# Kernel tuning notes

Hardware: AMD Instinct MI355X
Metric: run time of the kernel (lower is better)

Reference implementation:

```python
import jax, jax.numpy as jnp
import numpy as np

PRE = 2000          # pre_wbf_detections
POST = 300          # post_wbf_detections
IOU_THRESH = 0.55   # wbf_iou_thresh
NUM_CLASSES = 5


def setup_inputs() -> dict:
    key = jax.random.key(0)
    k1, k2, k3, k4 = jax.random.split(key, 4)
    # realistic xyxy boxes in a 1024px image
    ctr = jax.random.uniform(k1, (PRE, 2), minval=0.0, maxval=1024.0)
    wh = jax.random.uniform(k2, (PRE, 2), minval=8.0, maxval=96.0)
    boxes = jnp.concatenate([ctr - wh / 2, ctr + wh / 2], axis=1)
    scores = jax.random.uniform(k3, (PRE, 1), minval=0.05, maxval=1.0)
    labels = jax.random.randint(k4, (PRE, 1), 0, NUM_CLASSES).astype(jnp.float32)
    x = jnp.concatenate([boxes, scores, labels], axis=1)  # (PRE, 6)
    return {"x": x}


def _iou_one_vs_many(box, mboxes):
    # torchvision-style box_iou of one box (4,) vs many (N,4)
    lt = jnp.maximum(box[:2], mboxes[:, :2])
    rb = jnp.minimum(box[2:], mboxes[:, 2:])
    wh = jnp.clip(rb - lt, 0.0)
    inter = wh[:, 0] * wh[:, 1]
    a1 = (box[2] - box[0]) * (box[3] - box[1])
    a2 = (mboxes[:, 2] - mboxes[:, 0]) * (mboxes[:, 3] - mboxes[:, 1])
    union = a1 + a2 - inter
    safe = jnp.where(union > 0, union, 1.0)
    return jnp.where(union > 0, inter / safe, 0.0)


def _wbf_forward(x):
    # Sequential WBF clustering. The torch code runs wbf() per unique class;
    # since a detection can only join a cluster of its own class and cluster
    # creation order within a class is preserved, a single sequential pass
    # with a class-equality check is mathematically identical (final result
    # is sorted by score, so per-class concatenation order is irrelevant).
    N = x.shape[0]
    # cluster state: score-weighted box sum, score sum, member count, class, valid
    init = (
        jnp.zeros((N, 4), x.dtype),   # sum of score*box per cluster
        jnp.zeros((N,), x.dtype),     # sum of scores per cluster
        jnp.zeros((N,), jnp.int32),   # member count per cluster
        jnp.zeros((N,), x.dtype),     # class id per cluster
        jnp.zeros((N,), bool),        # cluster slot valid
    )

    def step(carry, det):
        sum_wb, sum_s, cnt, cls, valid = carry
        box, score, c = det[:4], det[4], det[5]
        denom = jnp.where(valid, sum_s, 1.0)
        mboxes = sum_wb / denom[:, None]  # current merged boxes
        iou = _iou_one_vs_many(box, mboxes)
        match = valid & (cls == c) & (iou > IOU_THRESH)
        found = jnp.any(match)
        first = jnp.argmax(match)                  # first matching cluster
        n_valid = jnp.sum(valid).astype(jnp.int32)  # next free slot
        idx = jnp.where(found, first, n_valid)
        sum_wb = sum_wb.at[idx].add(score * box)
        sum_s = sum_s.at[idx].add(score)
        cnt = cnt.at[idx].add(1)
        cls = cls.at[idx].set(c)
        valid = valid.at[idx].set(True)
        return (sum_wb, sum_s, cnt, cls, valid), None

    (sum_wb, sum_s, cnt, cls, valid), _ = jax.lax.scan(step, init, x)

    denom = jnp.where(valid, sum_s, 1.0)
    boxes = sum_wb / denom[:, None]                              # weighted avg box
    scores = sum_s / jnp.maximum(cnt.astype(x.dtype), 1.0)       # mean score
    sort_key = jnp.where(valid, scores, -1.0)
    order = jnp.argsort(-sort_key)                               # descending by score
    top = order[:POST]
    vtop = valid[top]
    out = jnp.concatenate(
        [boxes[top], scores[top, None], cls[top, None]], axis=1)  # (POST, 6)
    return jnp.where(vtop[:, None], out, 0.0)


def reference(x):
    return _wbf_forward(x[:PRE])
```

## Files before the change

kernel.cpp:

```cpp
#include <hip/hip_runtime.h>

typedef unsigned long long u64;
typedef unsigned short u16;
typedef unsigned u32;
typedef unsigned char u8;

#define PRE   2000
#define POST  300
#define NCLS  5
#define CAP   512
#define INF   0x7fffffff
#define SORTG 8

#define MID 0x1.19999A8p-1

template <int K> struct IC { static constexpr int v = K; };
template <int N, typename F> __device__ __forceinline__ void unrollN(F&& f) {
    if constexpr (N > 0) { unrollN<N - 1>(f); f(IC<N - 1>{}); }
}

__device__ __forceinline__ float rlF(float v, int l) {
    return __uint_as_float((u32)__builtin_amdgcn_readlane((int)__float_as_uint(v), l));
}

__device__ __forceinline__ bool iou_pred(float bx0, float bx1, float bx2, float bx3,
                                         float a1, float m0, float m1, float m2, float m3,
                                         float a2) {
    const float ltx = fmaxf(bx0, m0), lty = fmaxf(bx1, m1);
    const float rbx = fminf(bx2, m2), rby = fminf(bx3, m3);
    const float wd = fmaxf(rbx - ltx, 0.f), hg = fmaxf(rby - lty, 0.f);
    const float inter = wd * hg;
    const float uni = (a1 + a2) - inter;
    return (uni > 0.f) && ((double)inter >= MID * (double)uni);
}

__device__ __forceinline__ u64 mk_key(float sc, int g, int id) {
    return ~(((u64)__float_as_uint(sc) << 32) |
             ((u64)(unsigned)(0xFFFF - g) << 16) | (u64)id);
}

__global__ __launch_bounds__(512, 1) void wbf_matrix(const float* __restrict__ x,
                                                     u64* __restrict__ M,
                                                     float* __restrict__ dets,
                                                     int* __restrict__ nlist,
                                                     u64* __restrict__ keysg,
                                                     u32* __restrict__ histg) {
#pragma clang fp contract(off)
    __shared__ int s_wc[8];
    __shared__ u16 s_list[CAP];

    const int tid  = threadIdx.x;
    const int lane = tid & 63;
    const int wave = tid >> 6;
    const int b    = blockIdx.x;
    const int cls  = b >> 4;
    const float mycls = (float)cls;

    if (b == 1) for (int i = tid; i < NCLS * CAP; i += 512) keysg[i] = ~0ull;
    if (b == 2) for (int i = tid; i < 4096; i += 512) histg[i] = 0u;

    u64 wm[4]; int wcnt = 0;
    const int tb = wave * 256;
    #pragma unroll
    for (int i = 0; i < 4; ++i) {
        const int t = tb + i * 64 + lane;
        const bool pp = (t < PRE) && (x[t * 6 + 5] == mycls);
        wm[i] = __ballot(pp);
        wcnt += (int)__popcll(wm[i]);
    }
    if (lane == 0) s_wc[wave] = wcnt;
    __syncthreads();
    int off = 0, tot = 0;
    #pragma unroll
    for (int w = 0; w < 8; ++w) {
        const int cw = s_wc[w];
        off += (w < wave) ? cw : 0;
        tot += cw;
    }
    #pragma unroll
    for (int i = 0; i < 4; ++i) {
        const int t = tb + i * 64 + lane;
        const bool pp = ((wm[i] >> lane) & 1ull) != 0ull;
        const int pos = off + (int)__popcll(wm[i] & (((u64)1 << lane) - 1ull));
        if (pp && pos < CAP) s_list[pos] = (u16)t;
        off += (int)__popcll(wm[i]);
    }
    const int myn = (tot > CAP) ? CAP : tot;
    __syncthreads();

    {
        float qc0[8], qc1[8], qc2[8], qc3[8], ac[8];
        unrollN<8>([&](auto k_) {
            constexpr int K = decltype(k_)::v;
            const int c = K * 64 + lane;
            qc0[K] = 0.f; qc1[K] = 0.f; qc2[K] = 0.f; qc3[K] = 0.f; ac[K] = 0.f;
            if (c < myn) {
                const int g = s_list[c];
                const float* p = x + g * 6;
                const float b0 = p[0], b1 = p[1], b2 = p[2], b3 = p[3], sc = p[4];
                qc0[K] = (sc * b0) / sc; qc1[K] = (sc * b1) / sc;
                qc2[K] = (sc * b2) / sc; qc3[K] = (sc * b3) / sc;
                ac[K] = (qc2[K] - qc0[K]) * (qc3[K] - qc1[K]);
            }
        });
        const int slice = (b & 15) * 8 + wave;
        const int rlo = slice * 4;
        const int rhi = (rlo + 4 < myn) ? rlo + 4 : myn;
        const int nr = rhi - rlo;
        if (nr > 0) {
            float rv0 = 0.f, rv1 = 0.f, rv2 = 0.f, rv3 = 0.f;
            if (lane < nr) {
                const int g = s_list[rlo + lane];
                const float* p = x + g * 6;
                rv0 = p[0]; rv1 = p[1]; rv2 = p[2]; rv3 = p[3];
            }
            for (int i = 0; i < nr; ++i) {
                const int r = rlo + i;
                const float bx0 = rlF(rv0, i), bx1 = rlF(rv1, i);
                const float bx2 = rlF(rv2, i), bx3 = rlF(rv3, i);
                const float a1 = (bx2 - bx0) * (bx3 - bx1);
                const int Wmax = r >> 6;
                unrollN<8>([&](auto w_) {
                    constexpr int W = decltype(w_)::v;
                    if (W <= Wmax) {
                        const int c = W * 64 + lane;
                        const bool pred = (c < r) &&
                            iou_pred(bx0, bx1, bx2, bx3, a1, qc0[W], qc1[W], qc2[W], qc3[W], ac[W]);
                        const u64 bits = __ballot(pred);
                        if (lane == 0) M[((size_t)(cls * CAP + r)) * 8 + W] = bits;
                    }
                });
            }
        }
    }

    if ((b & 15) == 0) {
        for (int rr = tid; rr < myn; rr += 512) {
            const int g = s_list[rr];
            const float* p = x + g * 6;
            const float b0 = p[0], b1 = p[1], b2 = p[2], b3 = p[3], sc = p[4];
            float* dr = dets + (size_t)(cls * CAP + rr) * 8;
            dr[0] = b0; dr[1] = b1; dr[2] = b2; dr[3] = b3;
            dr[4] = sc; dr[5] = (b2 - b0) * (b3 - b1);
            ((int*)dr)[6] = g; ((int*)dr)[7] = 0;
        }
        if (tid == 0) nlist[cls] = myn;
    }
}

__global__ __launch_bounds__(512, 1) void wbf_scan(const u64* __restrict__ M,
                                                   const float* __restrict__ dets,
                                                   const int* __restrict__ nlist,
                                                   float* __restrict__ recs,
                                                   int* __restrict__ cnts,
                                                   u64* __restrict__ keysg,
                                                   u32* __restrict__ histg) {
#pragma clang fp contract(off)
    __shared__ __align__(16) char s_buf[57408];
    u8*  s_mtx = (u8*)s_buf;
    float (*s_det)[8]  = (float (*)[8])(s_buf + 32768);
    float (*s_dov)[16] = (float (*)[16])(s_buf + 49152);
    u8*  s_ab          = (u8*)(s_buf + 57344);

    const int tid  = threadIdx.x;
    const int lane = tid & 63;
    const int wave = tid >> 6;
    const int cls  = blockIdx.x;

    const int myn = nlist[cls];

    {
        const ulonglong2* Mg = (const ulonglong2*)(M + (size_t)cls * CAP * 8);
        ulonglong2* Ml = (ulonglong2*)s_mtx;
        const int nit = myn * 4;
        for (int it = tid; it < nit; it += 512) Ml[it] = Mg[it];
    }
    {
        const float4* Dg = (const float4*)(dets + (size_t)cls * CAP * 8);
        float4* Dl = (float4*)s_det;
        const int nit = myn * 2;
        for (int it = tid; it < nit; it += 512) Dl[it] = Dg[it];
    }
    if (tid < 64) s_ab[tid] = 0;
    __syncthreads();
    if (wave != 0) return;

    u32 aliveB = 0;
    int dirtyCnt = 0;
    bool consA = false;
    int resCode = 0, resIdx = 0;
    float dR0 = 0.f, dR1 = 0.f, dR2 = 0.f, dR3 = 0.f, dRa = 0.f;
    float dS0 = 0.f, dS1 = 0.f, dS2 = 0.f, dS3 = 0.f, dSs = 0.f;
    int dRank = INF, dGi = 0, dCnt = 0;
    float rm0 = 0.f, rm1 = 0.f, rm2 = 0.f, rm3 = 0.f, rma = 0.f;

    auto resolve = [&](int r, float bx0, float bx1, float bx2, float bx3,
                       float sc, float a1, u32 rowByte, u64 balC) {
        const u32 mC = rowByte & aliveB;
        int rank_c = INF;
        if (balC) {
            const int wl = (int)__builtin_ctzll(balC);
            const u32 byte = (u32)__builtin_amdgcn_readlane((int)mC, wl);
            rank_c = wl * 8 + (int)__builtin_ctz(byte);
        }
        const int rcs = (rank_c == INF) ? 0 : rank_c;
        const float4 cbv = *(const float4*)&s_det[rcs][0];
        const float4 cbe = *(const float4*)&s_det[rcs][4];
        const float cb0 = cbv.x, cb1 = cbv.y, cb2 = cbv.z, cb3 = cbv.w;
        const float csc = cbe.x;
        const int cgi = __float_as_int(cbe.z);

        int rank_d = INF, di = -1;
        if (dirtyCnt > 0) {
            const int DN = (dirtyCnt < 64) ? dirtyCnt : 64;
            const bool p = (lane < DN) &&
                iou_pred(bx0, bx1, bx2, bx3, a1, dR0, dR1, dR2, dR3, dRa);
            const int myrk = p ? dRank : INF;
            u64 mk = __ballot(p);
            while (mk) {
                const int l = (int)__builtin_ctzll(mk);
                mk &= mk - 1;
                const int rk = __builtin_amdgcn_readlane(myrk, l);
                if (rk < rank_d) { rank_d = rk; di = l; }
            }
            const int DH2 = (dirtyCnt < 128) ? dirtyCnt : 128;
            for (int dd = 64; dd < DH2; ++dd) {
                const float* dv = s_dov[dd];
                if (iou_pred(bx0, bx1, bx2, bx3, a1, dv[0], dv[1], dv[2], dv[3], dv[4])) {
                    const int rk = ((const int*)dv)[10];
                    if (rk < rank_d) { rank_d = rk; di = dd; }
                }
            }
        }
        if (rank_c == INF && rank_d == INF) {
            aliveB |= ((r >> 3) == lane) ? (1u << (r & 7)) : 0u;
            resCode = 0;
        } else if (rank_c < rank_d) {
            const int rc = rank_c;
            aliveB &= ~(((rc >> 3) == lane) ? (1u << (rc & 7)) : 0u);
            const float ns0 = (csc * cb0) + sc * bx0;
            const float ns1 = (csc * cb1) + sc * bx1;
            const float ns2 = (csc * cb2) + sc * bx2;
            const float ns3 = (csc * cb3) + sc * bx3;
            const float nss = csc + sc;
            const float nm0 = ns0 / nss, nm1 = ns1 / nss;
            const float nm2 = ns2 / nss, nm3 = ns3 / nss;
            const float nar = (nm2 - nm0) * (nm3 - nm1);
            const int D = dirtyCnt;
            if (D < 64) {
                if (lane == D) {
                    dR0 = nm0; dR1 = nm1; dR2 = nm2; dR3 = nm3; dRa = nar;
                    dS0 = ns0; dS1 = ns1; dS2 = ns2; dS3 = ns3; dSs = nss;
                    dRank = rc; dGi = cgi; dCnt = 2;
                }
            } else if (D < 128) {
                if (lane == 0) {
                    float* dv = s_dov[D];
                    dv[0] = nm0; dv[1] = nm1; dv[2] = nm2; dv[3] = nm3; dv[4] = nar;
                    dv[5] = ns0; dv[6] = ns1; dv[7] = ns2; dv[8] = ns3; dv[9] = nss;
                    ((int*)dv)[10] = rc; ((int*)dv)[11] = cgi; ((int*)dv)[12] = 2;
                }
            }
            dirtyCnt++;
            resCode = 1; resIdx = D;
            rm0 = nm0; rm1 = nm1; rm2 = nm2; rm3 = nm3; rma = nar;
        } else {
            float f0, f1, f2, f3, fs; int nct;
            if (di < 64) {
                f0 = rlF(dS0, di) + sc * bx0; f1 = rlF(dS1, di) + sc * bx1;
                f2 = rlF(dS2, di) + sc * bx2; f3 = rlF(dS3, di) + sc * bx3;
                fs = rlF(dSs, di) + sc;
                nct = __builtin_amdgcn_readlane(dCnt, di) + 1;
            } else {
                const float* dv = s_dov[di];
                f0 = dv[5] + sc * bx0; f1 = dv[6] + sc * bx1;
                f2 = dv[7] + sc * bx2; f3 = dv[8] + sc * bx3;
                fs = dv[9] + sc;
                nct = ((const int*)dv)[12] + 1;
            }
            const float nm0 = f0 / fs, nm1 = f1 / fs, nm2 = f2 / fs, nm3 = f3 / fs;
            const float nar = (nm2 - nm0) * (nm3 - nm1);
            if (di < 64) {
                if (lane == di) {
                    dR0 = nm0; dR1 = nm1; dR2 = nm2; dR3 = nm3; dRa = nar;
                    dS0 = f0; dS1 = f1; dS2 = f2; dS3 = f3; dSs = fs; dCnt = nct;
                }
            } else {
                if (lane == 0) {
                    float* dw = s_dov[di];
                    dw[0] = nm0; dw[1] = nm1; dw[2] = nm2; dw[3] = nm3; dw[4] = nar;
                    dw[5] = f0; dw[6] = f1; dw[7] = f2; dw[8] = f3; dw[9] = fs;
                    ((int*)dw)[12] = nct;
                }
            }
            rm0 = nm0; rm1 = nm1; rm2 = nm2; rm3 = nm3; rma = nar;
            resCode = 2; resIdx = di;
        }
    };

    for (int K8 = 0; K8 < 8; ++K8) {
        const int r0 = K8 * 64;
        if (r0 >= myn) break;
        const int cnt = (myn - r0 < 64) ? (myn - r0) : 64;
        const bool valid = lane < cnt;
        const u64 validM = (cnt == 64) ? ~0ull : (((u64)1 << cnt) - 1ull);
        u64 orv = 0ull;
        {
            const int rr = r0 + (valid ? lane : 0);
            const u64* rp = (const u64*)&s_mtx[(size_t)rr * 64];
            const u64* av = (const u64*)s_ab;
            #pragma unroll
            for (int W = 0; W < 8; ++W) {
                if (W <= K8) {
                    const u64 msk = (W == K8) ? ~0ull : av[W];
                    orv |= rp[W] & msk;
                }
            }
        }
        const u64 rowW = __ballot(valid && orv != 0ull);
        float4 db = make_float4(0.f, 0.f, 0.f, 0.f);
        float2 de = make_float2(1.f, 0.f);
        if (valid) {
            db = *(const float4*)&s_det[r0 + lane][0];
            de = *(const float2*)&s_det[r0 + lane][4];
        }
        u64 dmaskLo = 0ull, dmaskHi = 0ull;
        if (!consA) {
            const int DN = (dirtyCnt < 64) ? dirtyCnt : 64;
            for (int d = 0; d < DN; ++d) {
                const float m0 = rlF(dR0, d), m1 = rlF(dR1, d);
                const float m2 = rlF(dR2, d), m3 = rlF(dR3, d);
                const float ma = rlF(dRa, d);
                const bool pp = valid && iou_pred(db.x, db.y, db.z, db.w, de.y,
                                                 m0, m1, m2, m3, ma);
                if (pp) dmaskLo |= 1ull << d;
            }
            const int DH = (dirtyCnt < 128) ? dirtyCnt : 128;
            for (int dd = 64; dd < DH; ++dd) {
                const float* dv = s_dov[dd];
                const bool pp = valid && iou_pred(db.x, db.y, db.z, db.w, de.y,
                                                 dv[0], dv[1], dv[2], dv[3], dv[4]);
                if (pp) dmaskHi |= 1ull << (dd - 64);
            }
        }
        u64 danyb = __ballot((dmaskLo | dmaskHi) != 0ull);

        u32 prB[8]; int prP[8];
        {
            u64 t = consA ? validM : ((danyb | rowW) & validM);
            #pragma unroll
            for (int i = 0; i < 8; ++i) {
                const int f = t ? (int)__builtin_ctzll(t) : 0;
                prP[i] = t ? f : 64;
                prB[i] = (u32)s_mtx[(size_t)(r0 + f) * 64 + lane];
                t &= t - 1ull;
            }
        }

        int p = 0;
        while (p < cnt) {
            u64 vm = consA ? validM : ((danyb | rowW) & validM);
            vm &= ~(((u64)1 << p) - 1ull);
            const int F = vm ? (int)__builtin_ctzll(vm) : cnt;
            {
                const int lo = r0 + p, h2 = r0 + F;
                int s = lo - 8 * lane; s = (s > 0) ? s : 0;
                int e = h2 - 8 * lane; e = (e < 8) ? e : 8;
                if (e > s) aliveB |= ((0xFFu >> (8 - (e - s))) << s);
            }
            s_ab[lane] = (u8)aliveB;
            if (F >= cnt) break;
            const int r = r0 + F;
            u32 rowByte = 0u; bool hit = false;
            #pragma unroll
            for (int i = 0; i < 8; ++i)
                if (prP[i] == F) { rowByte = prB[i]; hit = true; }
            if (!hit) rowByte = (u32)s_mtx[(size_t)r * 64 + lane];
            const u64 balCq = __ballot((rowByte & aliveB) != 0u);
            const bool Fdirty = consA || (((danyb >> F) & 1ull) != 0ull);
            if (!Fdirty && balCq == 0ull) {
                aliveB |= ((r >> 3) == lane) ? (1u << (r & 7)) : 0u;
                s_ab[lane] = (u8)aliveB;
            } else {
                const float bx0 = rlF(db.x, F), bx1 = rlF(db.y, F);
                const float bx2 = rlF(db.z, F), bx3 = rlF(db.w, F);
                const float sc = rlF(de.x, F), a1 = rlF(de.y, F);
                resolve(r, bx0, bx1, bx2, bx3, sc, a1, rowByte, balCq);
                s_ab[lane] = (u8)aliveB;
                if (resCode != 0) {
                    const int idx = resIdx;
                    if (idx < 128) {
                        const bool pnew = valid && (lane > F) &&
                            iou_pred(db.x, db.y, db.z, db.w, de.y,
                                     rm0, rm1, rm2, rm3, rma);
                        const u64 nb = __ballot(pnew);
                        const u64 bit = (nb >> lane) & 1ull;
                        if (idx < 64)
                            dmaskLo = (dmaskLo & ~(1ull << idx)) | (bit << idx);
                        else
                            dmaskHi = (dmaskHi & ~(1ull << (idx - 64))) | (bit << (idx - 64));
                        danyb = __ballot((dmaskLo | dmaskHi) != 0ull);
                    } else {
                        consA = true;
                    }
                }
            }
            p = F + 1;
        }
    }

    int wo = 0;
    for (int Kw = 0; Kw < 8; ++Kw) {
        u64 am = 0ull;
        #pragma unroll
        for (int bb = 0; bb < 8; ++bb)
            am |= (u64)(u32)(u8)__builtin_amdgcn_readlane((int)aliveB, Kw * 8 + bb) << (8 * bb);
        const int j = Kw * 64 + lane;
        const bool pred = (am >> lane) & 1ull;
        if (pred) {
            const int pos = wo + (int)__popcll(am & (((u64)1 << lane) - 1));
            const float b0 = s_det[j][0], b1 = s_det[j][1];
            const float b2 = s_det[j][2], b3 = s_det[j][3];
            const float sc = s_det[j][4];
            const int g = ((const int*)s_det[j])[6];
            const int id = cls * CAP + pos;
            float* rec = recs + (size_t)id * 8;
            rec[0] = (sc * b0) / sc; rec[1] = (sc * b1) / sc;
            rec[2] = (sc * b2) / sc; rec[3] = (sc * b3) / sc;
            rec[4] = sc;
            ((int*)rec)[5] = g;
            const u64 skey = mk_key(sc, g, id);
            keysg[id] = skey;
            atomicAdd(&histg[(u32)(skey >> 52)], 1u);
        }
        wo += (int)__popcll(am);
    }
    const int demit = (dirtyCnt < 128) ? dirtyCnt : 128;
    {
        const int dreg = (demit < 64) ? demit : 64;
        if (lane < dreg) {
            const int id = cls * CAP + wo + lane;
            float* rec = recs + (size_t)id * 8;
            const float scd = dSs / (float)dCnt;
            rec[0] = dR0; rec[1] = dR1; rec[2] = dR2; rec[3] = dR3;
            rec[4] = scd;
            ((int*)rec)[5] = dGi;
            const u64 skey = mk_key(scd, dGi, id);
            keysg[id] = skey;
            atomicAdd(&histg[(u32)(skey >> 52)], 1u);
        }
        for (int d = 64 + lane; d < demit; d += 64) {
            const float* dv = s_dov[d];
            const int id = cls * CAP + wo + d;
            float* rec = recs + (size_t)id * 8;
            const float scd = dv[9] / (float)(((const int*)dv)[12]);
            const int g = ((const int*)dv)[11];
            rec[0] = dv[0]; rec[1] = dv[1]; rec[2] = dv[2]; rec[3] = dv[3];
            rec[4] = scd;
            ((int*)rec)[5] = g;
            const u64 skey = mk_key(scd, g, id);
            keysg[id] = skey;
            atomicAdd(&histg[(u32)(skey >> 52)], 1u);
        }
    }
    if (lane == 0) cnts[cls] = wo + demit;
}

__global__ __launch_bounds__(512, 1) void wbf_sort(const u64* __restrict__ keysg,
                                                   const u32* __restrict__ histg,
                                                   const float* __restrict__ recs,
                                                   const int* __restrict__ cnts,
                                                   float* __restrict__ out) {
    __shared__ __align__(16) char s_buf[28864];
    u64* keysL   = (u64*)s_buf;
    u64* cand    = (u64*)(s_buf + 20480);
    u32* partial = (u32*)(s_buf + 24576);
    u32* part    = (u32*)(s_buf + 26624);
    int* wcnt    = (int*)(s_buf + 26656);
    int* scal    = (int*)(s_buf + 26688);

    const int tid  = threadIdx.x;
    const int lane = tid & 63;
    const int wave = tid >> 6;
    const int g    = blockIdx.x;

    if (tid == 0) { scal[0] = 0; scal[1] = 0; }

    int n = 0;
    #pragma unroll
    for (int w = 0; w < NCLS; ++w) n += cnts[w];
    const int target = (POST < n) ? POST : n;

    u32 p = 0;
    #pragma unroll
    for (int k = 0; k < 8; ++k) p += histg[tid * 8 + k];
    u32 v = p;
    #pragma unroll
    for (int o2 = 1; o2 < 64; o2 <<= 1) {
        const u32 t = (u32)__shfl_up((int)v, o2);
        if (lane >= o2) v += t;
    }
    if (lane == 63) part[wave] = v;
    __syncthreads();
    u32 base = 0;
    #pragma unroll
    for (int w = 0; w < 8; ++w) base += (w < wave) ? part[w] : 0u;
    const u32 I = base + v;
    const u32 E = I - p;
    if ((int)E < target && (int)I >= target) { scal[0] = tid; scal[1] = (int)E; }
    __syncthreads();
    const int T = scal[0];
    int cum = scal[1];
    int B = T * 8 + 7;
    for (int bb = T * 8; bb < T * 8 + 8; ++bb) {
        const int h = (int)histg[bb];
        if (cum + h >= target) { B = bb; break; }
        cum += h;
    }
    const int candCount = cum + (int)histg[B];

    if (candCount <= 512) {
        int running = 0;
        #pragma unroll
        for (int c5 = 0; c5 < 5; ++c5) {
            const u64 kk = keysg[c5 * 512 + tid];
            const bool pred = ((u32)(kk >> 52) <= (u32)B);
            const u64 m = __ballot(pred);
            if (lane == 0) wcnt[wave] = (int)__popcll(m);
            __syncthreads();
            int wb = running;
            #pragma unroll
            for (int w = 0; w < 8; ++w) {
                wb += (w < wave) ? wcnt[w] : 0;
                running += wcnt[w];
            }
            if (pred)
                cand[wb + (int)__popcll(m & (((u64)1 << lane) - 1ull))] = kk;
            __syncthreads();
        }
        if (tid >= candCount) cand[tid] = (~0ull << 16) | (u64)(0xF000u + tid);
        __syncthreads();

        const u64 kc = cand[g * 64 + lane];
        int pc = 0;
        #pragma unroll 8
        for (int j = 0; j < 64; ++j) {
            const u64 kj = cand[wave * 64 + j];
            pc += (int)(kj < kc);
        }
        partial[wave * 64 + lane] = (u32)pc;
        __syncthreads();
        if (wave == 0) {
            int rk = 0;
            #pragma unroll
            for (int w = 0; w < 8; ++w) rk += (int)partial[w * 64 + lane];
            if (rk < target) {
                const u64 key = ~kc;
                const int id = (int)(key & 0xFFFFull);
                const float* rec = recs + (size_t)id * 8;
                float* o = out + rk * 6;
                o[0] = rec[0]; o[1] = rec[1]; o[2] = rec[2]; o[3] = rec[3];
                o[4] = __uint_as_float((unsigned)(key >> 32));
                o[5] = (float)(id >> 9);
            }
        }
        if (g == 0 && tid >= target && tid < POST) {
            float* o = out + tid * 6;
            o[0] = 0.f; o[1] = 0.f; o[2] = 0.f; o[3] = 0.f; o[4] = 0.f; o[5] = 0.f;
        }
    } else {
        if (g != 0) return;
        for (int i = tid; i < NCLS * CAP; i += 512) keysL[i] = keysg[i];
        __syncthreads();
        u64 myk5[5]; int rk5[5];
        #pragma unroll
        for (int s = 0; s < 5; ++s) { myk5[s] = keysL[s * 512 + tid]; rk5[s] = 0; }
        for (int j = 0; j < NCLS * CAP; ++j) {
            const u64 kj = keysL[j];
            #pragma unroll
            for (int s = 0; s < 5; ++s)
                rk5[s] += (int)((kj < myk5[s]) || (kj == myk5[s] && j < s * 512 + tid));
        }
        #pragma unroll
        for (int s = 0; s < 5; ++s) {
            const int rk = rk5[s];
            if (rk < target) {
                const u64 key = ~myk5[s];
                const int id = (int)(key & 0xFFFFull);
                const float* rec = recs + (size_t)id * 8;
                float* o = out + rk * 6;
                o[0] = rec[0]; o[1] = rec[1]; o[2] = rec[2]; o[3] = rec[3];
                o[4] = __uint_as_float((unsigned)(key >> 32));
                o[5] = (float)(id >> 9);
            }
        }
        if (tid >= target && tid < POST) {
            float* o = out + tid * 6;
            o[0] = 0.f; o[1] = 0.f; o[2] = 0.f; o[3] = 0.f; o[4] = 0.f; o[5] = 0.f;
        }
    }
}

extern "C" void kernel_launch(void* const* d_in, const int* in_sizes, int n_in,
                              void* d_out, int out_size, void* d_ws, size_t ws_size,
                              hipStream_t stream) {
    const float* x = (const float*)d_in[0];
    float* out = (float*)d_out;
    u64*   M     = (u64*)d_ws;
    float* dets  = (float*)((char*)d_ws + 163840);
    float* recs  = (float*)((char*)d_ws + 245760);
    int*   cnts  = (int*)((char*)d_ws + 327680);
    int*   nlist = cnts + 16;
    u64*   keysg = (u64*)((char*)d_ws + 327936);
    u32*   histg = (u32*)((char*)d_ws + 348416);
    wbf_matrix<<<NCLS * 16, 512, 0, stream>>>(x, M, dets, nlist, keysg, histg);
    wbf_scan<<<NCLS, 512, 0, stream>>>(M, dets, nlist, recs, cnts, keysg, histg);
    wbf_sort<<<SORTG, 512, 0, stream>>>(keysg, histg, recs, cnts, out);
}
```

Measured before the change: 92.07 us.

## Fuse sort kernel into scan kernel via atomic completion counter

Drops the separate sort launch by appending SORTG extra blocks to the scan grid. These blocks spin on an agent-scope acquire counter that each class block increments with a release after finishing. The goal is to remove one kernel launch and its gap. Separately, the per-iteration shared-memory store of the alive byte is moved out of the inner loop to a single store after it. This relies on all 13 blocks being co-resident to avoid deadlock, and the spinning blocks occupy CUs while they wait.

```diff
diff --git a/kernel.cpp b/kernel.cpp
--- a/kernel.cpp
+++ b/kernel.cpp
@@ -17,6 +17,10 @@
 template <int K> struct IC { static constexpr int v = K; };
 template <int N, typename F> __device__ __forceinline__ void unrollN(F&& f) {
     if constexpr (N > 0) { unrollN<N - 1>(f); f(IC<N - 1>{}); }
+}
+
+__device__ __forceinline__ u32 aload_acq(u32* p) {
+    return __hip_atomic_load(p, __ATOMIC_ACQUIRE, __HIP_MEMORY_SCOPE_AGENT);
 }
 
 __device__ __forceinline__ float rlF(float v, int l) {
@@ -44,7 +48,8 @@
                                                      float* __restrict__ dets,
                                                      int* __restrict__ nlist,
                                                      u64* __restrict__ keysg,
-                                                     u32* __restrict__ histg) {
+                                                     u32* __restrict__ histg,
+                                                     u32* __restrict__ ctrl) {
 #pragma clang fp contract(off)
     __shared__ int s_wc[8];
     __shared__ u16 s_list[CAP];
@@ -58,6 +63,7 @@
 
     if (b == 1) for (int i = tid; i < NCLS * CAP; i += 512) keysg[i] = ~0ull;
     if (b == 2) for (int i = tid; i < 4096; i += 512) histg[i] = 0u;
+    if (b == 3 && tid == 0) ctrl[0] = 0u;
 
     u64 wm[4]; int wcnt = 0;
     const int tb = wave * 256;
@@ -154,18 +160,151 @@
                                                    float* __restrict__ recs,
                                                    int* __restrict__ cnts,
                                                    u64* __restrict__ keysg,
-                                                   u32* __restrict__ histg) {
+                                                   u32* __restrict__ histg,
+                                                   u32* __restrict__ ctrl,
+                                                   float* __restrict__ out) {
 #pragma clang fp contract(off)
     __shared__ __align__(16) char s_buf[57408];
+
+    const int tid  = threadIdx.x;
+    const int lane = tid & 63;
+    const int wave = tid >> 6;
+    const int cls  = blockIdx.x;
+
+    if (cls >= NCLS) {
+        u64* keysL   = (u64*)s_buf;
+        u64* cand    = (u64*)(s_buf + 20480);
+        u32* partial = (u32*)(s_buf + 24576);
+        u32* part    = (u32*)(s_buf + 26624);
+        int* wcnt    = (int*)(s_buf + 26656);
+        int* scal    = (int*)(s_buf + 26688);
+
+        const int g = cls - NCLS;
+
+        if (tid == 0) { while (aload_acq(&ctrl[0]) < (u32)NCLS) {} }
+        __syncthreads();
+        if (tid == 0) { scal[0] = 0; scal[1] = 0; }
+
+        int n = 0;
+        #pragma unroll
+        for (int w = 0; w < NCLS; ++w) n += cnts[w];
+        const int target = (POST < n) ? POST : n;
+
+        u32 p = 0;
+        #pragma unroll
+        for (int k = 0; k < 8; ++k) p += histg[tid * 8 + k];
+        u32 v = p;
+        #pragma unroll
+        for (int o2 = 1; o2 < 64; o2 <<= 1) {
+            const u32 t = (u32)__shfl_up((int)v, o2);
+            if (lane >= o2) v += t;
+        }
+        if (lane == 63) part[wave] = v;
+        __syncthreads();
+        u32 base = 0;
+        #pragma unroll
+        for (int w = 0; w < 8; ++w) base += (w < wave) ? part[w] : 0u;
+        const u32 I = base + v;
+        const u32 E = I - p;
+        if ((int)E < target && (int)I >= target) { scal[0] = tid; scal[1] = (int)E; }
+        __syncthreads();
+        const int T = scal[0];
+        int cum = scal[1];
+        int B = T * 8 + 7;
+        for (int bb = T * 8; bb < T * 8 + 8; ++bb) {
+            const int h = (int)histg[bb];
+            if (cum + h >= target) { B = bb; break; }
+            cum += h;
+        }
+        const int candCount = cum + (int)histg[B];
+
+        if (candCount <= 512) {
+            int running = 0;
+            #pragma unroll
+            for (int c5 = 0; c5 < 5; ++c5) {
+                const u64 kk = keysg[c5 * 512 + tid];
+                const bool pred = ((u32)(kk >> 52) <= (u32)B);
+                const u64 m = __ballot(pred);
+                if (lane == 0) wcnt[wave] = (int)__popcll(m);
+                __syncthreads();
+                int wb = running;
+                #pragma unroll
+                for (int w = 0; w < 8; ++w) {
+                    wb += (w < wave) ? wcnt[w] : 0;
+                    running += wcnt[w];
+                }
+                if (pred)
+                    cand[wb + (int)__popcll(m & (((u64)1 << lane) - 1ull))] = kk;
+                __syncthreads();
+            }
+            if (tid >= candCount) cand[tid] = (~0ull << 16) | (u64)(0xF000u + tid);
+            __syncthreads();
+
+            const u64 kc = cand[g * 64 + lane];
+            int pc = 0;
+            #pragma unroll 8
+            for (int j = 0; j < 64; ++j) {
+                const u64 kj = cand[wave * 64 + j];
+                pc += (int)(kj < kc);
+            }
+            partial[wave * 64 + lane] = (u32)pc;
+            __syncthreads();
+            if (wave == 0) {
+                int rk = 0;
+                #pragma unroll
+                for (int w = 0; w < 8; ++w) rk += (int)partial[w * 64 + lane];
+                if (rk < target) {
+                    const u64 key = ~kc;
+                    const int id = (int)(key & 0xFFFFull);
+                    const float* rec = recs + (size_t)id * 8;
+                    float* o = out + rk * 6;
+                    o[0] = rec[0]; o[1] = rec[1]; o[2] = rec[2]; o[3] = rec[3];
+                    o[4] = __uint_as_float((unsigned)(key >> 32));
+                    o[5] = (float)(id >> 9);
+                }
+            }
+            if (g == 0 && tid >= target && tid < POST) {
+                float* o = out + tid * 6;
+                o[0] = 0.f; o[1] = 0.f; o[2] = 0.f; o[3] = 0.f; o[4] = 0.f; o[5] = 0.f;
+            }
+        } else {
+            if (g != 0) return;
+            for (int i = tid; i < NCLS * CAP; i += 512) keysL[i] = keysg[i];
+            __syncthreads();
+            u64 myk5[5]; int rk5[5];
+            #pragma unroll
+            for (int s = 0; s < 5; ++s) { myk5[s] = keysL[s * 512 + tid]; rk5[s] = 0; }
+            for (int j = 0; j < NCLS * CAP; ++j) {
+                const u64 kj = keysL[j];
+                #pragma unroll
+                for (int s = 0; s < 5; ++s)
+                    rk5[s] += (int)((kj < myk5[s]) || (kj == myk5[s] && j < s * 512 + tid));
+            }
+            #pragma unroll
+            for (int s = 0; s < 5; ++s) {
+                const int rk = rk5[s];
+                if (rk < target) {
+                    const u64 key = ~myk5[s];
+                    const int id = (int)(key & 0xFFFFull);
+                    const float* rec = recs + (size_t)id * 8;
+                    float* o = out + rk * 6;
+                    o[0] = rec[0]; o[1] = rec[1]; o[2] = rec[2]; o[3] = rec[3];
+                    o[4] = __uint_as_float((unsigned)(key >> 32));
+                    o[5] = (float)(id >> 9);
+                }
+            }
+            if (tid >= target && tid < POST) {
+                float* o = out + tid * 6;
+                o[0] = 0.f; o[1] = 0.f; o[2] = 0.f; o[3] = 0.f; o[4] = 0.f; o[5] = 0.f;
+            }
+        }
+        return;
+    }
+
     u8*  s_mtx = (u8*)s_buf;
     float (*s_det)[8]  = (float (*)[8])(s_buf + 32768);
     float (*s_dov)[16] = (float (*)[16])(s_buf + 49152);
     u8*  s_ab          = (u8*)(s_buf + 57344);
-
-    const int tid  = threadIdx.x;
-    const int lane = tid & 63;
-    const int wave = tid >> 6;
-    const int cls  = blockIdx.x;
 
     const int myn = nlist[cls];
 
@@ -368,7 +507,6 @@
                 int e = h2 - 8 * lane; e = (e < 8) ? e : 8;
                 if (e > s) aliveB |= ((0xFFu >> (8 - (e - s))) << s);
             }
-            s_ab[lane] = (u8)aliveB;
             if (F >= cnt) break;
             const int r = r0 + F;
             u32 rowByte = 0u; bool hit = false;
@@ -380,13 +518,11 @@
             const bool Fdirty = consA || (((danyb >> F) & 1ull) != 0ull);
             if (!Fdirty && balCq == 0ull) {
                 aliveB |= ((r >> 3) == lane) ? (1u << (r & 7)) : 0u;
-                s_ab[lane] = (u8)aliveB;
             } else {
                 const float bx0 = rlF(db.x, F), bx1 = rlF(db.y, F);
                 const float bx2 = rlF(db.z, F), bx3 = rlF(db.w, F);
                 const float sc = rlF(de.x, F), a1 = rlF(de.y, F);
                 resolve(r, bx0, bx1, bx2, bx3, sc, a1, rowByte, balCq);
-                s_ab[lane] = (u8)aliveB;
                 if (resCode != 0) {
                     const int idx = resIdx;
                     if (idx < 128) {
@@ -407,6 +543,7 @@
             }
             p = F + 1;
         }
+        s_ab[lane] = (u8)aliveB;
     }
 
     int wo = 0;
@@ -464,141 +601,9 @@
         }
     }
     if (lane == 0) cnts[cls] = wo + demit;
-}
-
-__global__ __launch_bounds__(512, 1) void wbf_sort(const u64* __restrict__ keysg,
-                                                   const u32* __restrict__ histg,
-                                                   const float* __restrict__ recs,
-                                                   const int* __restrict__ cnts,
-                                                   float* __restrict__ out) {
-    __shared__ __align__(16) char s_buf[28864];
-    u64* keysL   = (u64*)s_buf;
-    u64* cand    = (u64*)(s_buf + 20480);
-    u32* partial = (u32*)(s_buf + 24576);
-    u32* part    = (u32*)(s_buf + 26624);
-    int* wcnt    = (int*)(s_buf + 26656);
-    int* scal    = (int*)(s_buf + 26688);
-
-    const int tid  = threadIdx.x;
-    const int lane = tid & 63;
-    const int wave = tid >> 6;
-    const int g    = blockIdx.x;
-
-    if (tid == 0) { scal[0] = 0; scal[1] = 0; }
-
-    int n = 0;
-    #pragma unroll
-    for (int w = 0; w < NCLS; ++w) n += cnts[w];
-    const int target = (POST < n) ? POST : n;
-
-    u32 p = 0;
-    #pragma unroll
-    for (int k = 0; k < 8; ++k) p += histg[tid * 8 + k];
-    u32 v = p;
-    #pragma unroll
-    for (int o2 = 1; o2 < 64; o2 <<= 1) {
-        const u32 t = (u32)__shfl_up((int)v, o2);
-        if (lane >= o2) v += t;
-    }
-    if (lane == 63) part[wave] = v;
-    __syncthreads();
-    u32 base = 0;
-    #pragma unroll
-    for (int w = 0; w < 8; ++w) base += (w < wave) ? part[w] : 0u;
-    const u32 I = base + v;
-    const u32 E = I - p;
-    if ((int)E < target && (int)I >= target) { scal[0] = tid; scal[1] = (int)E; }
-    __syncthreads();
-    const int T = scal[0];
-    int cum = scal[1];
-    int B = T * 8 + 7;
-    for (int bb = T * 8; bb < T * 8 + 8; ++bb) {
-        const int h = (int)histg[bb];
-        if (cum + h >= target) { B = bb; break; }
-        cum += h;
-    }
-    const int candCount = cum + (int)histg[B];
-
-    if (candCount <= 512) {
-        int running = 0;
-        #pragma unroll
-        for (int c5 = 0; c5 < 5; ++c5) {
-            const u64 kk = keysg[c5 * 512 + tid];
-            const bool pred = ((u32)(kk >> 52) <= (u32)B);
-            const u64 m = __ballot(pred);
-            if (lane == 0) wcnt[wave] = (int)__popcll(m);
-            __syncthreads();
-            int wb = running;
-            #pragma unroll
-            for (int w = 0; w < 8; ++w) {
-                wb += (w < wave) ? wcnt[w] : 0;
-                running += wcnt[w];
-            }
-            if (pred)
-                cand[wb + (int)__popcll(m & (((u64)1 << lane) - 1ull))] = kk;
-            __syncthreads();
-        }
-        if (tid >= candCount) cand[tid] = (~0ull << 16) | (u64)(0xF000u + tid);
-        __syncthreads();
-
-        const u64 kc = cand[g * 64 + lane];
-        int pc = 0;
-        #pragma unroll 8
-        for (int j = 0; j < 64; ++j) {
-            const u64 kj = cand[wave * 64 + j];
-            pc += (int)(kj < kc);
-        }
-        partial[wave * 64 + lane] = (u32)pc;
-        __syncthreads();
-        if (wave == 0) {
-            int rk = 0;
-            #pragma unroll
-            for (int w = 0; w < 8; ++w) rk += (int)partial[w * 64 + lane];
-            if (rk < target) {
-                const u64 key = ~kc;
-                const int id = (int)(key & 0xFFFFull);
-                const float* rec = recs + (size_t)id * 8;
-                float* o = out + rk * 6;
-                o[0] = rec[0]; o[1] = rec[1]; o[2] = rec[2]; o[3] = rec[3];
-                o[4] = __uint_as_float((unsigned)(key >> 32));
-                o[5] = (float)(id >> 9);
-            }
-        }
-        if (g == 0 && tid >= target && tid < POST) {
-            float* o = out + tid * 6;
-            o[0] = 0.f; o[1] = 0.f; o[2] = 0.f; o[3] = 0.f; o[4] = 0.f; o[5] = 0.f;
-        }
-    } else {
-        if (g != 0) return;
-        for (int i = tid; i < NCLS * CAP; i += 512) keysL[i] = keysg[i];
-        __syncthreads();
-        u64 myk5[5]; int rk5[5];
-        #pragma unroll
-        for (int s = 0; s < 5; ++s) { myk5[s] = keysL[s * 512 + tid]; rk5[s] = 0; }
-        for (int j = 0; j < NCLS * CAP; ++j) {
-            const u64 kj = keysL[j];
-            #pragma unroll
-            for (int s = 0; s < 5; ++s)
-                rk5[s] += (int)((kj < myk5[s]) || (kj == myk5[s] && j < s * 512 + tid));
-        }
-        #pragma unroll
-        for (int s = 0; s < 5; ++s) {
-            const int rk = rk5[s];
-            if (rk < target) {
-                const u64 key = ~myk5[s];
-                const int id = (int)(key & 0xFFFFull);
-                const float* rec = recs + (size_t)id * 8;
-                float* o = out + rk * 6;
-                o[0] = rec[0]; o[1] = rec[1]; o[2] = rec[2]; o[3] = rec[3];
-                o[4] = __uint_as_float((unsigned)(key >> 32));
-                o[5] = (float)(id >> 9);
-            }
-        }
-        if (tid >= target && tid < POST) {
-            float* o = out + tid * 6;
-            o[0] = 0.f; o[1] = 0.f; o[2] = 0.f; o[3] = 0.f; o[4] = 0.f; o[5] = 0.f;
-        }
-    }
+    __threadfence();
+    if (lane == 0)
+        __hip_atomic_fetch_add(&ctrl[0], 1u, __ATOMIC_RELEASE, __HIP_MEMORY_SCOPE_AGENT);
 }
 
 extern "C" void kernel_launch(void* const* d_in, const int* in_sizes, int n_in,
@@ -613,7 +618,8 @@
     int*   nlist = cnts + 16;
     u64*   keysg = (u64*)((char*)d_ws + 327936);
     u32*   histg = (u32*)((char*)d_ws + 348416);
-    wbf_matrix<<<NCLS * 16, 512, 0, stream>>>(x, M, dets, nlist, keysg, histg);
-    wbf_scan<<<NCLS, 512, 0, stream>>>(M, dets, nlist, recs, cnts, keysg, histg);
-    wbf_sort<<<SORTG, 512, 0, stream>>>(keysg, histg, recs, cnts, out);
-}
+    u32*   ctrl  = (u32*)((char*)d_ws + 364800);
+    wbf_matrix<<<NCLS * 16, 512, 0, stream>>>(x, M, dets, nlist, keysg, histg, ctrl);
+    wbf_scan<<<NCLS + SORTG, 512, 0, stream>>>(M, dets, nlist, recs, cnts, keysg,
+                                               histg, ctrl, out);
+}
```

Measured after the change: 92.23 us. No clear change (+0.2%).
